# Kernel tuning notes

Measured on AMD Instinct MI355X. Metric: run time of the kernel, lower is better.

## Reference

```python
import jax, jax.numpy as jnp
import numpy as np

D = 256   # koopman_dim
B = 256   # batch of initial latent states
T_STEPS = 512
DT = 0.01


def setup_inputs() -> dict:
    key = jax.random.key(0)
    k1, k2 = jax.random.split(key)
    z0 = jax.random.normal(k1, (B, D), dtype=jnp.float32)
    # nnx.Linear default lecun_normal init: std ~ 1/sqrt(fan_in)
    kernel = jax.random.normal(k2, (D, D), dtype=jnp.float32) / jnp.sqrt(jnp.float32(D))
    log_dt = jnp.asarray(jnp.log(DT), dtype=jnp.float32)
    return {"z0": z0, "kernel": kernel, "log_dt": log_dt, "T": T_STEPS}


def reference(z0, kernel, log_dt, T):
    dt = jnp.exp(log_dt)
    eye = jnp.eye(kernel.shape[0], dtype=kernel.dtype)
    # Bilinear / Tustin discretization: K_d = (I - 0.5*dt*K)^-1 (I + 0.5*dt*K)
    K_discrete = jnp.linalg.solve(eye - 0.5 * dt * kernel, eye + 0.5 * dt * kernel)

    def step(z, _):
        z_next = z @ K_discrete  # [B, D] @ [D, D]
        return z_next, z_next

    _, preds = jax.lax.scan(step, z0, None, length=T)  # preds: [T, B, D]
    return jnp.transpose(preds, (1, 0, 2))  # [B, T, D]
```

## Files before the change

kernel.cpp:

```cpp
#include <hip/hip_runtime.h>


#define DD 256
#define TT 512
#define MATF (DD * DD)
#define LDT ((size_t)TT * (size_t)DD)

typedef __attribute__((ext_vector_type(8))) short bf16x8;
typedef __attribute__((ext_vector_type(4))) float f32x4;

#define GLD16(g, l)                                                  \
    __builtin_amdgcn_global_load_lds(                                \
        (const __attribute__((address_space(1))) void*)(g),          \
        (__attribute__((address_space(3))) void*)(l), 16, 0, 0)

static __device__ __forceinline__ unsigned short f2bf(float f) {
    unsigned int u = __float_as_uint(f);
    u += 0x7fffu + ((u >> 16) & 1u);
    return (unsigned short)(u >> 16);
}
static __device__ __forceinline__ unsigned pack2bf(float a, float b) {
    return (unsigned)f2bf(a) | ((unsigned)f2bf(b) << 16);
}

__device__ __forceinline__ void g32_core(const float* __restrict__ Ab, int lda,
                                         const float* __restrict__ Bb, int ldb,
                                         int rowBase, int colBase, float acc[2][2]) {
    __shared__ __align__(16) float As[64 * 38];
    __shared__ __align__(16) float Bs[64 * 40];
    const int tid = threadIdx.x;
    const int tx = tid & 15, ty = tid >> 4;
    const int am = tid >> 4;
    const int ak = (tid & 15) << 2;
    const int bk = tid >> 3;
    const int bn = (tid & 7) << 2;

    acc[0][0] = acc[0][1] = acc[1][0] = acc[1][1] = 0.f;

    float4 pa0 = *(const float4*)(Ab + (size_t)(rowBase + am) * lda + ak);
    float4 pa1 = *(const float4*)(Ab + (size_t)(rowBase + am + 16) * lda + ak);
    float4 pb0 = *(const float4*)(Bb + (size_t)bk * ldb + colBase + bn);
    float4 pb1 = *(const float4*)(Bb + (size_t)(bk + 32) * ldb + colBase + bn);

    for (int k0 = 0; k0 < DD; k0 += 64) {
        As[(ak + 0) * 38 + am] = pa0.x;
        As[(ak + 1) * 38 + am] = pa0.y;
        As[(ak + 2) * 38 + am] = pa0.z;
        As[(ak + 3) * 38 + am] = pa0.w;
        As[(ak + 0) * 38 + am + 16] = pa1.x;
        As[(ak + 1) * 38 + am + 16] = pa1.y;
        As[(ak + 2) * 38 + am + 16] = pa1.z;
        As[(ak + 3) * 38 + am + 16] = pa1.w;
        *(float4*)(&Bs[bk * 40 + bn]) = pb0;
        *(float4*)(&Bs[(bk + 32) * 40 + bn]) = pb1;
        __syncthreads();
        if (k0 + 64 < DD) {
            pa0 = *(const float4*)(Ab + (size_t)(rowBase + am) * lda + k0 + 64 + ak);
            pa1 = *(const float4*)(Ab + (size_t)(rowBase + am + 16) * lda + k0 + 64 + ak);
            pb0 = *(const float4*)(Bb + (size_t)(bk + k0 + 64) * ldb + colBase + bn);
            pb1 = *(const float4*)(Bb + (size_t)(bk + 32 + k0 + 64) * ldb + colBase + bn);
        }
#pragma unroll
        for (int kk = 0; kk < 64; ++kk) {
            float2 a2 = *(const float2*)(&As[kk * 38 + (ty << 1)]);
            float2 b2 = *(const float2*)(&Bs[kk * 40 + (tx << 1)]);
            acc[0][0] = fmaf(a2.x, b2.x, acc[0][0]);
            acc[0][1] = fmaf(a2.x, b2.y, acc[0][1]);
            acc[1][0] = fmaf(a2.y, b2.x, acc[1][0]);
            acc[1][1] = fmaf(a2.y, b2.y, acc[1][1]);
        }
        __syncthreads();
    }
}

__global__ void __launch_bounds__(256)
p1_kernel(const float* __restrict__ K, float* __restrict__ Pw) {
    {
        int b = ((blockIdx.y * 8 + blockIdx.x) * 256 + threadIdx.x) * 4;
        *(float4*)(Pw + b) = *(const float4*)(K + b);
    }
    float acc[2][2];
    const int rowBase = blockIdx.y << 5, colBase = blockIdx.x << 5;
    g32_core(K, DD, K, DD, rowBase, colBase, acc);
    float* Cb = Pw + MATF;
    const int r0 = rowBase + ((threadIdx.x >> 4) << 1);
    const int c0 = colBase + ((threadIdx.x & 15) << 1);
#pragma unroll
    for (int i = 0; i < 2; ++i) {
        int r = r0 + i;
        *(float2*)(Cb + (size_t)r * DD + c0) = (float2){acc[i][0], acc[i][1]};
    }
}

__global__ void __launch_bounds__(256)
gpow_kernel(const float* __restrict__ A, const float* __restrict__ B,
            float* __restrict__ C, long long sA, long long sB, long long sC) {
    float acc[2][2];
    const int rowBase = blockIdx.y << 5, colBase = blockIdx.x << 5;
    g32_core(A + blockIdx.z * sA, DD, B + blockIdx.z * sB, DD, rowBase, colBase, acc);
    float* Cb = C + blockIdx.z * sC;
    const int r0 = rowBase + ((threadIdx.x >> 4) << 1);
    const int c0 = colBase + ((threadIdx.x & 15) << 1);
#pragma unroll
    for (int i = 0; i < 2; ++i) {
        int r = r0 + i;
        *(float2*)(Cb + (size_t)r * DD + c0) = (float2){acc[i][0], acc[i][1]};
    }
}

__global__ void __launch_bounds__(256)
gpow4_kernel(float* __restrict__ Pw) {
    static const int sa[4] = {1, 2, 2, 3};
    static const int sb[4] = {2, 2, 3, 3};
    static const int sc[4] = {4, 5, 6, 7};
    const int z = blockIdx.z;
    float acc[2][2];
    const int rowBase = blockIdx.y << 5, colBase = blockIdx.x << 5;
    g32_core(Pw + (size_t)sa[z] * MATF, DD, Pw + (size_t)sb[z] * MATF, DD,
             rowBase, colBase, acc);
    float* Cb = Pw + (size_t)sc[z] * MATF;
    const int r0 = rowBase + ((threadIdx.x >> 4) << 1);
    const int c0 = colBase + ((threadIdx.x & 15) << 1);
#pragma unroll
    for (int i = 0; i < 2; ++i) {
        int r = r0 + i;
        *(float2*)(Cb + (size_t)r * DD + c0) = (float2){acc[i][0], acc[i][1]};
    }
}

__global__ void __launch_bounds__(256)
comb_kernel(const float* __restrict__ Pw, const float* __restrict__ log_dt,
            const float* __restrict__ z0, unsigned short* __restrict__ MTb,
            float* __restrict__ W1, float* __restrict__ W2,
            float* __restrict__ W3, unsigned short* __restrict__ Zb0) {
    __shared__ float tle[8][32][33];
    __shared__ float gtab[34][8];
    const int tid = threadIdx.x;
    const int k0 = blockIdx.y << 5, c0 = blockIdx.x << 5;
    const float csf = 0.5f * expf(log_dt[0]);

    {
        int b = ((blockIdx.y * 8 + blockIdx.x) * 256 + tid) * 4;
        uint2 w;
        w.x = pack2bf(z0[b], z0[b + 1]);
        w.y = pack2bf(z0[b + 2], z0[b + 3]);
        *(uint2*)(Zb0 + b) = w;
    }

    if (tid < 34) {
        int j = (tid < 32) ? (tid + 1) : ((tid == 32) ? 64 : 96);
        double b[9], cq[9];
        b[0] = 1.0;
        cq[0] = 1.0;
#pragma unroll
        for (int p = 1; p <= 8; ++p) {
            b[p] = b[p - 1] * (double)(j - p + 1) / (double)p;
            cq[p] = cq[p - 1] * (double)(j + p - 1) / (double)p;
        }
        double csm = (double)csf;
#pragma unroll
        for (int m = 1; m <= 8; ++m) {
            double s = 0.0;
#pragma unroll
            for (int p = 0; p <= 8; ++p)
                if (p <= m) s += b[p] * cq[m - p];
            gtab[tid][m - 1] = (float)(s * csm);
            csm *= (double)csf;
        }
    }

    const int ltx = tid & 31, lty = tid >> 5;
#pragma unroll
    for (int m = 0; m < 8; ++m)
#pragma unroll
        for (int it = 0; it < 4; ++it) {
            int k = lty + (it << 3);
            tle[m][ltx][k] =
                Pw[(size_t)m * MATF + (size_t)(k0 + k) * DD + c0 + ltx];
        }
    __syncthreads();

    const int c = tid >> 3;
    const int kb = (tid & 7) << 2;
    float em[8][4];
#pragma unroll
    for (int m = 0; m < 8; ++m)
#pragma unroll
        for (int u = 0; u < 4; ++u) em[m][u] = tle[m][c][kb + u];

    float diag[4];
#pragma unroll
    for (int u = 0; u < 4; ++u)
        diag[u] = ((k0 + kb + u) == (c0 + c)) ? 1.f : 0.f;

    float w32[4];
    for (int j = 1; j <= 32; ++j) {
        float val[4] = {diag[0], diag[1], diag[2], diag[3]};
        const float* gj = gtab[j - 1];
#pragma unroll
        for (int m = 0; m < 8; ++m)
#pragma unroll
            for (int u = 0; u < 4; ++u) val[u] = fmaf(gj[m], em[m][u], val[u]);
        uint2 w;
        w.x = pack2bf(val[0], val[1]);
        w.y = pack2bf(val[2], val[3]);
        *(uint2*)(MTb + (size_t)(j - 1) * MATF + (size_t)(c0 + c) * DD + k0 + kb) = w;
        if (j == 32) {
            w32[0] = val[0]; w32[1] = val[1]; w32[2] = val[2]; w32[3] = val[3];
        }
    }
    float w64[4] = {diag[0], diag[1], diag[2], diag[3]};
    float w96[4] = {diag[0], diag[1], diag[2], diag[3]};
#pragma unroll
    for (int m = 0; m < 8; ++m)
#pragma unroll
        for (int u = 0; u < 4; ++u) {
            w64[u] = fmaf(gtab[32][m], em[m][u], w64[u]);
            w96[u] = fmaf(gtab[33][m], em[m][u], w96[u]);
        }

    float* tw = &tle[0][0][0];
    const int wk = tid >> 3, wc = (tid & 7) << 2;
    float* Wd[3] = {W1, W2, W3};
    float* Ws[3] = {w32, w64, w96};
#pragma unroll
    for (int p = 0; p < 3; ++p) {
        __syncthreads();
#pragma unroll
        for (int u = 0; u < 4; ++u) tw[(kb + u) * 33 + c] = Ws[p][u];
        __syncthreads();
        float4 v = {tw[wk * 33 + wc], tw[wk * 33 + wc + 1],
                    tw[wk * 33 + wc + 2], tw[wk * 33 + wc + 3]};
        *(float4*)(Wd[p] + (size_t)(k0 + wk) * DD + c0 + wc) = v;
    }
}

__global__ void __launch_bounds__(256)
scan3_kernel(const float* __restrict__ z0, float* __restrict__ Zf,
             const float* __restrict__ W1, const float* __restrict__ W2,
             const float* __restrict__ W3, float* __restrict__ Wtab,
             unsigned short* __restrict__ Zb, int level) {
    static const signed char JA[3][7] = {{0, 0, 0, 17, 18, 0, 0},
                                         {0, 1, 2, 3, 2, 3, 20},
                                         {4, 5, 0, 1, 2, 3, 0}};
    static const signed char JB[3][7] = {{0, 1, 2, 1, 2, 0, 0},
                                         {3, 3, 3, 3, 4, 4, 4},
                                         {4, 4, 5, 5, 5, 5, 0}};
    static const signed char JD[3][7] = {{1, 2, 3, 19, 20, 0, 0},
                                         {4, 5, 6, 7, 8, 9, 21},
                                         {10, 11, 12, 13, 14, 15, 0}};
    const float* Wp[6] = {W1, W2, W3, Wtab, Wtab + MATF, Wtab + 2 * (size_t)MATF};
    const int jz = blockIdx.z;
    const int a = JA[level][jz], b = JB[level][jz], d = JD[level][jz];

    const float* Asrc;
    if (a == 0) Asrc = z0;
    else if (a < 16) Asrc = Zf + (size_t)a * MATF;
    else Asrc = Wp[a - 16];

    float acc[2][2];
    const int rowBase = blockIdx.y << 5, colBase = blockIdx.x << 5;
    g32_core(Asrc, DD, Wp[b], DD, rowBase, colBase, acc);

    const int r0 = rowBase + ((threadIdx.x >> 4) << 1);
    const int c0 = colBase + ((threadIdx.x & 15) << 1);
    if (d < 16) {
        float* Zo32 = Zf + (size_t)d * MATF;
        unsigned short* Zo = Zb + (size_t)d * MATF;
#pragma unroll
        for (int ii = 0; ii < 2; ++ii) {
            int r = r0 + ii;
            float2 v = {acc[ii][0], acc[ii][1]};
            *(float2*)(Zo32 + (size_t)r * DD + c0) = v;
            *(unsigned*)(Zo + (size_t)r * DD + c0) = pack2bf(v.x, v.y);
        }
    } else {
        float* Cb = Wtab + (size_t)(d - 19) * MATF;
#pragma unroll
        for (int ii = 0; ii < 2; ++ii) {
            int r = r0 + ii;
            *(float2*)(Cb + (size_t)r * DD + c0) = (float2){acc[ii][0], acc[ii][1]};
        }
    }
}

__global__ void __launch_bounds__(256)
fill_kernel(const unsigned short* __restrict__ Zb,
            const unsigned short* __restrict__ MTb,
            float* __restrict__ out) {
    __shared__ __align__(16) char pool[32768];
    const int zz = blockIdx.z;
    const int i = zz & 15;
    const int j = (zz >> 4) + 1;
    const int t = i * 32 + j - 1;
    const unsigned short* Zt = Zb + (size_t)i * MATF;
    const unsigned short* MT = MTb + (size_t)(j - 1) * MATF;

    const int tid = threadIdx.x;
    const int lane = tid & 63, wid = tid >> 6;
    const int rowBase = blockIdx.y * 128, colBase = blockIdx.x * 128;
    const int wr = (wid >> 1) * 64, wc = (wid & 1) * 64;

    int rowq[4], skq[4], ldsb[4];
#pragma unroll
    for (int q = 0; q < 4; ++q) {
        int c = q * 256 + wid * 64 + lane;
        int row = c >> 3;
        rowq[q] = row;
        skq[q] = ((c ^ (row & 7)) & 7) << 3;
        ldsb[q] = (q * 256 + wid * 64) << 4;
    }

    f32x4 acc[4][4];
#pragma unroll
    for (int a = 0; a < 4; ++a)
#pragma unroll
        for (int b = 0; b < 4; ++b) acc[a][b] = (f32x4){0.f, 0.f, 0.f, 0.f};

    auto stage = [&](int k0) {
#pragma unroll
        for (int q = 0; q < 4; ++q) {
            GLD16(Zt + (size_t)(rowBase + rowq[q]) * DD + k0 + skq[q], pool + ldsb[q]);
            GLD16(MT + (size_t)(colBase + rowq[q]) * DD + k0 + skq[q],
                  pool + 16384 + ldsb[q]);
        }
    };

    stage(0);
    for (int r = 0; r < 4; ++r) {
        __syncthreads();
        const char* asb = pool;
        const char* bsb = pool + 16384;
#pragma unroll
        for (int ks = 0; ks < 2; ++ks) {
            bf16x8 af[4], bg[4];
            const int kk = ks * 32 + (lane >> 4) * 8;
#pragma unroll
            for (int f = 0; f < 4; ++f) {
                int rr = wr + f * 16 + (lane & 15);
                af[f] = *(const bf16x8*)(asb + ((rr * 128 + kk * 2) ^ ((rr & 7) << 4)));
                int cc = wc + f * 16 + (lane & 15);
                bg[f] = *(const bf16x8*)(bsb + ((cc * 128 + kk * 2) ^ ((cc & 7) << 4)));
            }
#pragma unroll
            for (int fr = 0; fr < 4; ++fr)
#pragma unroll
                for (int fc = 0; fc < 4; ++fc)
                    acc[fr][fc] = __builtin_amdgcn_mfma_f32_16x16x32_bf16(
                        af[fr], bg[fc], acc[fr][fc], 0, 0, 0);
        }
        __syncthreads();
        if (r < 3) stage((r + 1) * 64);
    }

    float* Cs = (float*)pool;
    float* C = out + (size_t)t * DD;
#pragma unroll
    for (int hp = 0; hp < 2; ++hp) {
        __syncthreads();
        if (wr == hp * 64) {
#pragma unroll
            for (int fr = 0; fr < 4; ++fr) {
#pragma unroll
                for (int fc = 0; fc < 4; ++fc) {
                    int ccol = wc + fc * 16 + (lane & 15);
#pragma unroll
                    for (int ii = 0; ii < 4; ++ii) {
                        int lr = fr * 16 + ((lane >> 4) << 2) + ii;
                        int csw = ccol ^ (((lr >> 2) & 1) << 4);
                        Cs[lr * 128 + csw] = acc[fr][fc][ii];
                    }
                }
            }
        }
        __syncthreads();
#pragma unroll
        for (int it = 0; it < 8; ++it) {
            int chunk = it * 256 + tid;
            int row = chunk >> 5;
            int c4 = (chunk & 31) << 2;
            int csw = c4 ^ (((row >> 2) & 1) << 4);
            float4 v = *(const float4*)(Cs + row * 128 + csw);
            *(float4*)(C + (size_t)(rowBase + hp * 64 + row) * LDT + colBase + c4) = v;
        }
    }
}

__global__ void prep_kernel(const float* __restrict__ K,
                            const float* __restrict__ log_dt,
                            float* __restrict__ A) {
    int idx = blockIdx.x * blockDim.x + threadIdx.x;
    A[idx] = 0.5f * expf(log_dt[0]) * K[idx];
}

template <int EPI>
__global__ void __launch_bounds__(256)
g32_kernel(const float* A, const float* B, float* C, const float* E, float* C2,
           int lda, int ldb, int ldc, long long sA, long long sB, long long sC) {
    float acc[2][2];
    const int rowBase = blockIdx.y << 5, colBase = blockIdx.x << 5;
    g32_core(A + blockIdx.z * sA, lda, B + blockIdx.z * sB, ldb, rowBase, colBase, acc);
    float* Cb = C + blockIdx.z * sC;
    const int r0 = rowBase + ((threadIdx.x >> 4) << 1);
    const int c0 = colBase + ((threadIdx.x & 15) << 1);
#pragma unroll
    for (int i = 0; i < 2; ++i) {
        int r = r0 + i;
        float2 v;
        if (EPI == 2) {
            float e0 = E[(size_t)r * DD + c0], e1 = E[(size_t)r * DD + c0 + 1];
            v.x = acc[i][0] + 2.f * e0 + (r == c0 ? 1.f : 0.f);
            v.y = acc[i][1] + 2.f * e1 + (r == c0 + 1 ? 1.f : 0.f);
        } else {
            v.x = acc[i][0];
            v.y = acc[i][1];
        }
        *(float2*)(Cb + (size_t)r * ldc + c0) = v;
        if (EPI == 1) {
            float e0 = E[(size_t)r * DD + c0], e1 = E[(size_t)r * DD + c0 + 1];
            float2 w;
            w.x = 2.f * acc[i][0] + 2.f * e0 + (r == c0 ? 2.f : 0.f);
            w.y = 2.f * acc[i][1] + 2.f * e1 + (r == c0 + 1 ? 2.f : 0.f);
            *(float2*)(C2 + (size_t)r * DD + c0) = w;
        }
    }
}

extern "C" void kernel_launch(void* const* d_in, const int* in_sizes, int n_in,
                              void* d_out, int out_size, void* d_ws, size_t ws_size,
                              hipStream_t stream) {
    const float* z0 = (const float*)d_in[0];
    const float* Kmat = (const float*)d_in[1];
    const float* log_dt = (const float*)d_in[2];
    float* out = (float*)d_out;

    dim3 blk(256);

    float* Pw = (float*)d_ws;
    float* W1 = Pw + (size_t)8 * MATF;
    float* W2 = W1 + MATF;
    float* W3 = W2 + MATF;
    float* Wtab = W3 + MATF;
    float* Zf = Wtab + (size_t)3 * MATF;
    unsigned short* MTb = (unsigned short*)(Zf + (size_t)16 * MATF);
    unsigned short* Zb = MTb + (size_t)32 * MATF;
    const size_t need = (size_t)30 * MATF * 4 + (size_t)48 * MATF * 2;

    if (ws_size >= need) {
        dim3 g(8, 8, 1);
        p1_kernel<<<g, blk, 0, stream>>>(Kmat, Pw);
        gpow_kernel<<<dim3(8, 8, 2), blk, 0, stream>>>(
            Pw, Pw + MATF, Pw + 2 * (size_t)MATF, MATF, 0, MATF);
        gpow4_kernel<<<dim3(8, 8, 4), blk, 0, stream>>>(Pw);

        comb_kernel<<<g, blk, 0, stream>>>(Pw, log_dt, z0, MTb, W1, W2, W3, Zb);

        const int njobs[3] = {5, 7, 6};
        for (int s = 0; s < 3; ++s)
            scan3_kernel<<<dim3(8, 8, njobs[s]), blk, 0, stream>>>(
                z0, Zf, W1, W2, W3, Wtab, Zb, s);

        fill_kernel<<<dim3(2, 2, 512), blk, 0, stream>>>(Zb, MTb, out);
        return;
    }

    float* A = (float*)d_ws;
    float* A2f = A + MATF;
    float* Bopf = A2f + MATF;
    float* Kd = Bopf + MATF;
    prep_kernel<<<MATF / 256, blk, 0, stream>>>(Kmat, log_dt, A);
    dim3 g(8, 8, 1);
    g32_kernel<1><<<g, blk, 0, stream>>>(A, A, A2f, A, Bopf, DD, DD, DD, 0, 0, 0);
    g32_kernel<2><<<g, blk, 0, stream>>>(A2f, Bopf, Kd, A, (float*)0, DD, DD, DD, 0, 0, 0);
    for (int t = 0; t < TT; ++t) {
        const float* Ain = (t == 0) ? z0 : out + (size_t)(t - 1) * DD;
        int lda = (t == 0) ? DD : (int)LDT;
        g32_kernel<0><<<g, blk, 0, stream>>>(Ain, Kd, out + (size_t)t * DD,
                                             (const float*)0, (float*)0,
                                             lda, DD, (int)LDT, 0, 0, 0);
    }
}
```

Measured before the change: 103.3 us.

## Compute two extra 32-step powers in comb and cut scan to two levels

comb_kernel now also computes the matrix powers for 128 and 160 steps, giving five W matrices (W1..W5) instead of three. The three-level scan over the 16 chunk-start states becomes a two-level scan with wider job lists, 6 then 10 jobs. This removes one dependent kernel launch and shortens the serial chain. In exchange comb_kernel does more per-thread FMA work and makes two extra transposed stores. The workspace layout shifts, but the total size stays within the existing requirement.

```diff
diff --git a/kernel.cpp b/kernel.cpp
--- a/kernel.cpp
+++ b/kernel.cpp
@@ -132,9 +132,10 @@
 comb_kernel(const float* __restrict__ Pw, const float* __restrict__ log_dt,
             const float* __restrict__ z0, unsigned short* __restrict__ MTb,
             float* __restrict__ W1, float* __restrict__ W2,
-            float* __restrict__ W3, unsigned short* __restrict__ Zb0) {
+            float* __restrict__ W3, float* __restrict__ W4,
+            float* __restrict__ W5, unsigned short* __restrict__ Zb0) {
     __shared__ float tle[8][32][33];
-    __shared__ float gtab[34][8];
+    __shared__ float gtab[36][8];
     const int tid = threadIdx.x;
     const int k0 = blockIdx.y << 5, c0 = blockIdx.x << 5;
     const float csf = 0.5f * expf(log_dt[0]);
@@ -147,8 +148,8 @@
         *(uint2*)(Zb0 + b) = w;
     }
 
-    if (tid < 34) {
-        int j = (tid < 32) ? (tid + 1) : ((tid == 32) ? 64 : 96);
+    if (tid < 36) {
+        int j = (tid < 32) ? (tid + 1) : (32 * (tid - 30));
         double b[9], cq[9];
         b[0] = 1.0;
         cq[0] = 1.0;
@@ -209,22 +210,25 @@
             w32[0] = val[0]; w32[1] = val[1]; w32[2] = val[2]; w32[3] = val[3];
         }
     }
-    float w64[4] = {diag[0], diag[1], diag[2], diag[3]};
-    float w96[4] = {diag[0], diag[1], diag[2], diag[3]};
+    float wv[4][4];
+#pragma unroll
+    for (int q = 0; q < 4; ++q)
+#pragma unroll
+        for (int u = 0; u < 4; ++u) wv[q][u] = diag[u];
 #pragma unroll
     for (int m = 0; m < 8; ++m)
 #pragma unroll
-        for (int u = 0; u < 4; ++u) {
-            w64[u] = fmaf(gtab[32][m], em[m][u], w64[u]);
-            w96[u] = fmaf(gtab[33][m], em[m][u], w96[u]);
-        }
+        for (int q = 0; q < 4; ++q)
+#pragma unroll
+            for (int u = 0; u < 4; ++u)
+                wv[q][u] = fmaf(gtab[32 + q][m], em[m][u], wv[q][u]);
 
     float* tw = &tle[0][0][0];
     const int wk = tid >> 3, wc = (tid & 7) << 2;
-    float* Wd[3] = {W1, W2, W3};
-    float* Ws[3] = {w32, w64, w96};
-#pragma unroll
-    for (int p = 0; p < 3; ++p) {
+    float* Wd[5] = {W1, W2, W3, W4, W5};
+    float* Ws[5] = {w32, wv[0], wv[1], wv[2], wv[3]};
+#pragma unroll
+    for (int p = 0; p < 5; ++p) {
         __syncthreads();
 #pragma unroll
         for (int u = 0; u < 4; ++u) tw[(kb + u) * 33 + c] = Ws[p][u];
@@ -236,20 +240,21 @@
 }
 
 __global__ void __launch_bounds__(256)
-scan3_kernel(const float* __restrict__ z0, float* __restrict__ Zf,
+scan2_kernel(const float* __restrict__ z0, float* __restrict__ Zf,
              const float* __restrict__ W1, const float* __restrict__ W2,
-             const float* __restrict__ W3, float* __restrict__ Wtab,
+             const float* __restrict__ W3, const float* __restrict__ W4,
+             const float* __restrict__ W5, float* __restrict__ Wtab,
              unsigned short* __restrict__ Zb, int level) {
-    static const signed char JA[3][7] = {{0, 0, 0, 17, 18, 0, 0},
-                                         {0, 1, 2, 3, 2, 3, 20},
-                                         {4, 5, 0, 1, 2, 3, 0}};
-    static const signed char JB[3][7] = {{0, 1, 2, 1, 2, 0, 0},
-                                         {3, 3, 3, 3, 4, 4, 4},
-                                         {4, 4, 5, 5, 5, 5, 0}};
-    static const signed char JD[3][7] = {{1, 2, 3, 19, 20, 0, 0},
-                                         {4, 5, 6, 7, 8, 9, 21},
-                                         {10, 11, 12, 13, 14, 15, 0}};
-    const float* Wp[6] = {W1, W2, W3, Wtab, Wtab + MATF, Wtab + 2 * (size_t)MATF};
+    static const signed char JA[2][10] = {
+        {0, 0, 0, 0, 0, 20, 0, 0, 0, 0},
+        {1, 2, 3, 4, 5, 1, 2, 3, 4, 5}};
+    static const signed char JB[2][10] = {
+        {0, 1, 2, 3, 4, 4, 0, 0, 0, 0},
+        {4, 4, 4, 4, 4, 5, 5, 5, 5, 5}};
+    static const signed char JD[2][10] = {
+        {1, 2, 3, 4, 5, 19, 0, 0, 0, 0},
+        {6, 7, 8, 9, 10, 11, 12, 13, 14, 15}};
+    const float* Wp[6] = {W1, W2, W3, W4, W5, Wtab};
     const int jz = blockIdx.z;
     const int a = JA[level][jz], b = JB[level][jz], d = JD[level][jz];
 
@@ -275,7 +280,7 @@
             *(unsigned*)(Zo + (size_t)r * DD + c0) = pack2bf(v.x, v.y);
         }
     } else {
-        float* Cb = Wtab + (size_t)(d - 19) * MATF;
+        float* Cb = Wtab;
 #pragma unroll
         for (int ii = 0; ii < 2; ++ii) {
             int r = r0 + ii;
@@ -440,8 +445,10 @@
     float* W1 = Pw + (size_t)8 * MATF;
     float* W2 = W1 + MATF;
     float* W3 = W2 + MATF;
-    float* Wtab = W3 + MATF;
-    float* Zf = Wtab + (size_t)3 * MATF;
+    float* W4 = W3 + MATF;
+    float* W5 = W4 + MATF;
+    float* Wtab = W5 + MATF;
+    float* Zf = Wtab + MATF;
     unsigned short* MTb = (unsigned short*)(Zf + (size_t)16 * MATF);
     unsigned short* Zb = MTb + (size_t)32 * MATF;
     const size_t need = (size_t)30 * MATF * 4 + (size_t)48 * MATF * 2;
@@ -453,12 +460,13 @@
             Pw, Pw + MATF, Pw + 2 * (size_t)MATF, MATF, 0, MATF);
         gpow4_kernel<<<dim3(8, 8, 4), blk, 0, stream>>>(Pw);
 
-        comb_kernel<<<g, blk, 0, stream>>>(Pw, log_dt, z0, MTb, W1, W2, W3, Zb);
-
-        const int njobs[3] = {5, 7, 6};
-        for (int s = 0; s < 3; ++s)
-            scan3_kernel<<<dim3(8, 8, njobs[s]), blk, 0, stream>>>(
-                z0, Zf, W1, W2, W3, Wtab, Zb, s);
+        comb_kernel<<<g, blk, 0, stream>>>(Pw, log_dt, z0, MTb, W1, W2, W3, W4,
+                                           W5, Zb);
+
+        scan2_kernel<<<dim3(8, 8, 6), blk, 0, stream>>>(z0, Zf, W1, W2, W3, W4,
+                                                        W5, Wtab, Zb, 0);
+        scan2_kernel<<<dim3(8, 8, 10), blk, 0, stream>>>(z0, Zf, W1, W2, W3, W4,
+                                                         W5, Wtab, Zb, 1);
 
         fill_kernel<<<dim3(2, 2, 512), blk, 0, stream>>>(Zb, MTb, out);
         return;
```

Measured after the change: 96.80 us (median of 2 runs). 6.3% less time.
